# Kernel optimization log

Hardware: AMD Instinct MI355X
Metric: run time of the kernel (lower is better)

Reference implementation:

```python
import jax, jax.numpy as jnp
import numpy as np
import itertools

D_MODEL = 1024
TEMP = 0.3


def _hypercube(n):
    # all 2^n corners of {-1,+1}^n, matching generate_hypercube(n)
    return jnp.asarray(np.array(list(itertools.product([-1.0, 1.0], repeat=n)), dtype=np.float32))


def setup_inputs() -> dict:
    key = jax.random.key(0)
    ks = jax.random.split(key, 12)
    B, T, D = 8, 4096, D_MODEL
    s = 0.02
    return {
        "x": jax.random.normal(ks[0], (B, T, D), dtype=jnp.float32),
        "codes_l1": _hypercube(3),   # (8, 3)
        "codes_l2": _hypercube(6),   # (64, 6)
        "w_to_l1": jax.random.normal(ks[1], (D, 3), dtype=jnp.float32) * s,
        "w_from_l1": jax.random.normal(ks[2], (3, D), dtype=jnp.float32) * s,
        "w_to_l2": jax.random.normal(ks[3], (D, 6), dtype=jnp.float32) * s,
        "w_from_l2": jax.random.normal(ks[4], (6, D), dtype=jnp.float32) * s,
        "w_to_l3u": jax.random.normal(ks[5], (D, 6), dtype=jnp.float32) * s,
        "w_to_l3l": jax.random.normal(ks[6], (D, 6), dtype=jnp.float32) * s,
        "w_from_l3": jax.random.normal(ks[7], (12, D), dtype=jnp.float32) * s,
        "w_gate": jax.random.normal(ks[8], (D, 3), dtype=jnp.float32) * s,
        "b_gate": jnp.zeros((3,), dtype=jnp.float32),
        "temp_l1": jnp.log(jnp.float32(TEMP)),
        "temp_l2": jnp.log(jnp.float32(TEMP * 0.7)),
        "temp_l3": jnp.log(jnp.float32(TEMP * 0.5)),
        "scale_l1": jnp.float32(0.1),
        "scale_l2": jnp.float32(0.05),
        "scale_l3": jnp.float32(0.02),
    }


def _soft_quantize(z, codes, temp_log):
    # z: (B, T, n); codes: (K, n) -> (B, T, n)
    temp = jnp.clip(jnp.exp(temp_log), 0.01, 5.0)
    # Euclidean cdist: (B, T, K)
    dists = jnp.sqrt(jnp.sum(jnp.square(z[..., None, :] - codes), axis=-1))
    weights = jax.nn.softmax(-dists / temp, axis=-1)
    return weights @ codes


def reference(x, codes_l1, codes_l2, w_to_l1, w_from_l1, w_to_l2, w_from_l2,
              w_to_l3u, w_to_l3l, w_from_l3, w_gate, b_gate,
              temp_l1, temp_l2, temp_l3, scale_l1, scale_l2, scale_l3):
    # gate uses detached x
    gate = jax.nn.softmax(jax.lax.stop_gradient(x) @ w_gate + b_gate, axis=-1)  # (B,T,3)

    # Level 1: Z2^3
    q1 = _soft_quantize(x @ w_to_l1, codes_l1, temp_l1)
    out_l1 = q1 @ w_from_l1

    # Level 2: Z2^6
    q2 = _soft_quantize(x @ w_to_l2, codes_l2, temp_l2)
    out_l2 = q2 @ w_from_l2

    # Level 3: Z2^12 = two Z2^6 halves
    q3u = _soft_quantize(x @ w_to_l3u, codes_l2, temp_l3)
    q3l = _soft_quantize(x @ w_to_l3l, codes_l2, temp_l3)
    out_l3 = jnp.concatenate([q3u, q3l], axis=-1) @ w_from_l3

    out = (gate[..., 0:1] * scale_l1 * out_l1
           + gate[..., 1:2] * scale_l2 * out_l2
           + gate[..., 2:3] * scale_l3 * out_l3)
    gate_means = jnp.mean(gate, axis=(0, 1))  # stats dict analogue: (3,)
    return x + out, gate_means
```

## Files before the change

kernel.cpp:

```cpp
#include <hip/hip_runtime.h>
#include <stdint.h>


#define DM 1024
#define TPB 64
#define OUT_OFF ((size_t)33554432)
#define NTOK 32768
#define NSLOT 32
#define WSA_OFF 32768

typedef float f32x4 __attribute__((ext_vector_type(4)));
typedef short bf16x8 __attribute__((ext_vector_type(8)));

typedef const __attribute__((address_space(1))) unsigned int* gas1_t;
typedef __attribute__((address_space(3))) unsigned int* las3_t;

__device__ __forceinline__ void gl_lds16(const void* g, void* l){
  __builtin_amdgcn_global_load_lds((gas1_t)g, (las3_t)l, 16, 0, 0);
}

__device__ __forceinline__ short f2bf(float f){
  unsigned u = __builtin_bit_cast(unsigned, f);
  unsigned r = u + 0x7fffu + ((u >> 16) & 1u);
  return (short)(r >> 16);
}

template<int NB>
__device__ __forceinline__ void softq(const float* z, float invt, float* q){
  constexpr int K = 1 << NB;
  float d[K];
  float dmin = 3.4e38f;
#pragma unroll
  for (int j = 0; j < K; ++j){
    float acc = 0.f;
#pragma unroll
    for (int i = 0; i < NB; ++i){
      float c = ((j >> (NB-1-i)) & 1) ? 1.f : -1.f;
      float t = z[i] - c;
      acc = fmaf(t, t, acc);
    }
    float dj = sqrtf(acc);
    d[j] = dj;
    dmin = fminf(dmin, dj);
  }
  float S = 0.f;
  float s1[NB];
#pragma unroll
  for (int i = 0; i < NB; ++i) s1[i] = 0.f;
#pragma unroll
  for (int j = 0; j < K; ++j){
    float wj = __expf((dmin - d[j]) * invt);
    S += wj;
#pragma unroll
    for (int i = 0; i < NB; ++i)
      if ((j >> (NB-1-i)) & 1) s1[i] += wj;
  }
  float rS = 1.f / S;
#pragma unroll
  for (int i = 0; i < NB; ++i) q[i] = 2.f * s1[i] * rS - 1.f;
}

__global__ __launch_bounds__(256) void pack_kernel(
    const float* __restrict__ w_to_l1,  const float* __restrict__ w_to_l2,
    const float* __restrict__ w_to_l3u, const float* __restrict__ w_to_l3l,
    const float* __restrict__ w_gate,
    const float* __restrict__ w_from_l1, const float* __restrict__ w_from_l2,
    const float* __restrict__ w_from_l3,
    short* __restrict__ wsF, float* __restrict__ wsA)
{
  int base = blockIdx.x*4096 + threadIdx.x*16;
#pragma unroll
  for (int q = 0; q < 16; ++q){
    int e = base + q;
    float v;
    if (e < 32768){
      int s  = e >> 10;
      int nf = (e >> 9) & 1;
      int ll = (e >> 3) & 63;
      int j  = e & 7;
      int k  = s*32 + ((ll >> 4) << 3) + j;
      int n  = nf*16 + (ll & 15);
      if      (n < 3)  v = w_gate  [k*3 + n];
      else if (n < 6)  v = w_to_l1 [k*3 + (n-3)];
      else if (n < 12) v = w_to_l2 [k*6 + (n-6)];
      else if (n < 18) v = w_to_l3u[k*6 + (n-12)];
      else if (n < 24) v = w_to_l3l[k*6 + (n-18)];
      else             v = 0.f;
    } else {
      int e2  = e - 32768;
      int f   = e2 / 384;
      int rem = e2 - f*384;
      int ll  = rem >> 3;
      int j   = e2 & 7;
      int k   = ((ll >> 4) << 3) + j;
      int dd  = f*16 + (ll & 15);
      if      (k < 3)  v = w_from_l1[k*DM + dd];
      else if (k < 9)  v = w_from_l2[(k-3)*DM + dd];
      else if (k < 21) v = w_from_l3[(k-9)*DM + dd];
      else             v = 0.f;
    }
    wsF[e] = f2bf(v);
  }
  if (blockIdx.x == 0){
    wsA[threadIdx.x]       = 0.f;
    wsA[threadIdx.x + 256] = 0.f;
  }
}

__global__ __launch_bounds__(256, 2) void hq7_kernel(
    const float* __restrict__ x, const short* __restrict__ wsF,
    const float* __restrict__ b_gate,
    const float* __restrict__ t1p, const float* __restrict__ t2p, const float* __restrict__ t3p,
    const float* __restrict__ s1p, const float* __restrict__ s2p, const float* __restrict__ s3p,
    float* __restrict__ wsA, float* __restrict__ out)
{
  __shared__ alignas(16) char smem[80576];
  float* C   = reinterpret_cast<float*>(smem + 49152);
  float* P   = reinterpret_cast<float*>(smem + 66560);
  short* V16 = reinterpret_cast<short*>(smem + 75264);
  float* GS  = reinterpret_cast<float*>(smem + 80384);

  const int tid  = threadIdx.x;
  const int l    = tid & 63;
  const int wv   = tid >> 6;
  const int kg   = l >> 4;
  const int ln16 = l & 15;
  const int tb   = blockIdx.x * TPB;

  {
    f32x4 acc0 = {0.f,0.f,0.f,0.f}, acc1 = {0.f,0.f,0.f,0.f};
    const int lr0 = l >> 5;
    const int cbp = l & 31;
#pragma unroll
    for (int i = 0; i < 8; ++i){
      int lr = i*2 + lr0;
      gl_lds16(x + (size_t)(tb + wv*16 + lr)*DM + (cbp ^ (lr & 7))*4,
               smem + wv*16384 + i*1024 + l*16);
    }
#pragma unroll
    for (int t = 0; t < 8; ++t){
      const int buf = t & 1;
      bf16x8 bfr[8];
#pragma unroll
      for (int s2 = 0; s2 < 8; ++s2)
        bfr[s2] = *reinterpret_cast<const bf16x8*>(&wsF[(t*8 + s2)*512 + l*8]);
      __builtin_amdgcn_sched_barrier(0);
      if (t < 7){
#pragma unroll
        for (int i = 0; i < 8; ++i){
          int lr = i*2 + lr0;
          gl_lds16(x + (size_t)(tb + wv*16 + lr)*DM + (t+1)*128 + (cbp ^ (lr & 7))*4,
                   smem + wv*16384 + (buf^1)*8192 + i*1024 + l*16);
        }
        asm volatile("s_waitcnt vmcnt(8)" ::: "memory");
      } else {
        asm volatile("s_waitcnt vmcnt(0)" ::: "memory");
      }
      const char* abase = smem + wv*16384 + buf*8192 + ln16*512;
#pragma unroll
      for (int s = 0; s < 4; ++s){
        float4 xa = *reinterpret_cast<const float4*>(abase + ((s*8 + kg*2 + 0) ^ (ln16 & 7))*16);
        float4 xb = *reinterpret_cast<const float4*>(abase + ((s*8 + kg*2 + 1) ^ (ln16 & 7))*16);
        bf16x8 af;
        af[0]=f2bf(xa.x); af[1]=f2bf(xa.y); af[2]=f2bf(xa.z); af[3]=f2bf(xa.w);
        af[4]=f2bf(xb.x); af[5]=f2bf(xb.y); af[6]=f2bf(xb.z); af[7]=f2bf(xb.w);
        acc0 = __builtin_amdgcn_mfma_f32_16x16x32_bf16(af, bfr[s*2+0], acc0, 0, 0, 0);
        acc1 = __builtin_amdgcn_mfma_f32_16x16x32_bf16(af, bfr[s*2+1], acc1, 0, 0, 0);
      }
    }
#pragma unroll
    for (int r = 0; r < 4; ++r){
      int row = wv*16 + kg*4 + r;
      P[row*34 + ln16]      = acc0[r];
      P[row*34 + 16 + ln16] = acc1[r];
    }
  }
  __syncthreads();

  const short* wsFC = wsF + 32768;
  bf16x8 bwc0={0,0,0,0,0,0,0,0}, bwc1=bwc0, bwc2=bwc0, bwc3=bwc0;
  {
#pragma unroll
    for (int j = 0; j < 4; ++j){
      int lr = j*4 + (l >> 4);
      gl_lds16(x + (size_t)(tb + wv*16 + lr)*DM + ((l & 15) ^ (lr & 7))*4,
               smem + wv*12288 + j*1024 + l*16);
    }
    if (kg < 3){
      bwc0 = *reinterpret_cast<const bf16x8*>(&wsFC[(0*4+0)*384 + l*8]);
      bwc1 = *reinterpret_cast<const bf16x8*>(&wsFC[(0*4+1)*384 + l*8]);
      bwc2 = *reinterpret_cast<const bf16x8*>(&wsFC[(0*4+2)*384 + l*8]);
      bwc3 = *reinterpret_cast<const bf16x8*>(&wsFC[(0*4+3)*384 + l*8]);
    }
#pragma unroll
    for (int j = 0; j < 4; ++j){
      int lr = j*4 + (l >> 4);
      gl_lds16(x + (size_t)(tb + wv*16 + lr)*DM + 64 + ((l & 15) ^ (lr & 7))*4,
               smem + wv*12288 + 4096 + j*1024 + l*16);
    }
  }

  float qv[6] = {0,0,0,0,0,0};
  float myscale = 0.f;
  float sg0 = 0.f, sg1 = 0.f, sg2 = 0.f;
  {
    const int t = l;
    const int base = (wv == 3) ? 0 : 6 + wv*6;
    float z[6];
#pragma unroll
    for (int i = 0; i < 6; ++i) z[i] = P[t*34 + base + i];
    if (wv == 3){
      float invt1 = 1.f / fminf(fmaxf(__expf(t1p[0]), 0.01f), 5.0f);
      float g0l = z[0] + b_gate[0];
      float g1l = z[1] + b_gate[1];
      float g2l = z[2] + b_gate[2];
      float m  = fmaxf(g0l, fmaxf(g1l, g2l));
      float e0 = __expf(g0l - m), e1 = __expf(g1l - m), e2 = __expf(g2l - m);
      float rs = 1.f / (e0 + e1 + e2);
      float g0 = e0*rs, g1 = e1*rs, g2 = e2*rs;
      GS[t*3+0] = g0 * s1p[0];
      GS[t*3+1] = g1 * s2p[0];
      GS[t*3+2] = g2 * s3p[0];
      myscale   = g0 * s1p[0];
      float z1[3] = {z[3], z[4], z[5]};
      softq<3>(z1, invt1, qv);
      sg0 = g0; sg1 = g1; sg2 = g2;
#pragma unroll
      for (int mm = 1; mm < 64; mm <<= 1){
        sg0 += __shfl_xor(sg0, mm, 64);
        sg1 += __shfl_xor(sg1, mm, 64);
        sg2 += __shfl_xor(sg2, mm, 64);
      }
    } else {
      float tl = (wv == 0) ? t2p[0] : t3p[0];
      float invt = 1.f / fminf(fmaxf(__expf(tl), 0.01f), 5.0f);
      softq<6>(z, invt, qv);
    }
  }
  __syncthreads();

  {
    const int t = l;
    if (wv == 3){
#pragma unroll
      for (int i = 0; i < 3; ++i) V16[t*40 + i] = f2bf(myscale * qv[i]);
      V16[t*40 + 21] = 0; V16[t*40 + 22] = 0; V16[t*40 + 23] = 0;
    } else {
      float sc = GS[t*3 + ((wv == 0) ? 1 : 2)];
      int voff = 3 + wv*6;
#pragma unroll
      for (int i = 0; i < 6; ++i) V16[t*40 + voff + i] = f2bf(sc * qv[i]);
    }
  }
  __syncthreads();

  bf16x8 aV = {0,0,0,0,0,0,0,0};
  if (kg < 3)
    aV = *reinterpret_cast<const bf16x8*>(&V16[(wv*16 + ln16)*40 + kg*8]);
  const f32x4 z4 = {0.f,0.f,0.f,0.f};
  const int rl = l >> 2;
  const int cs = l & 3;

#pragma unroll
  for (int c = 0; c < 16; ++c){
    if (c == 0 || c == 15) asm volatile("s_waitcnt vmcnt(4)" ::: "memory");
    else                   asm volatile("s_waitcnt vmcnt(8)" ::: "memory");
    __builtin_amdgcn_sched_barrier(0);
    {
      f32x4 d0 = __builtin_amdgcn_mfma_f32_16x16x32_bf16(aV, bwc0, z4, 0, 0, 0);
      f32x4 d1 = __builtin_amdgcn_mfma_f32_16x16x32_bf16(aV, bwc1, z4, 0, 0, 0);
      f32x4 d2 = __builtin_amdgcn_mfma_f32_16x16x32_bf16(aV, bwc2, z4, 0, 0, 0);
      f32x4 d3 = __builtin_amdgcn_mfma_f32_16x16x32_bf16(aV, bwc3, z4, 0, 0, 0);
#pragma unroll
      for (int r = 0; r < 4; ++r){
        int rowb = (wv*16 + kg*4 + r)*68;
        C[rowb +  0 + ln16] = d0[r];
        C[rowb + 16 + ln16] = d1[r];
        C[rowb + 32 + ln16] = d2[r];
        C[rowb + 48 + ln16] = d3[r];
      }
    }
    __builtin_amdgcn_sched_barrier(0);
    bf16x8 bwn0 = bwc0, bwn1 = bwc1, bwn2 = bwc2, bwn3 = bwc3;
    if (c < 15 && kg < 3){
      bwn0 = *reinterpret_cast<const bf16x8*>(&wsFC[((c+1)*4+0)*384 + l*8]);
      bwn1 = *reinterpret_cast<const bf16x8*>(&wsFC[((c+1)*4+1)*384 + l*8]);
      bwn2 = *reinterpret_cast<const bf16x8*>(&wsFC[((c+1)*4+2)*384 + l*8]);
      bwn3 = *reinterpret_cast<const bf16x8*>(&wsFC[((c+1)*4+3)*384 + l*8]);
    }
    __builtin_amdgcn_sched_barrier(0);
    if (c < 14){
#pragma unroll
      for (int j = 0; j < 4; ++j){
        int lr = j*4 + (l >> 4);
        gl_lds16(x + (size_t)(tb + wv*16 + lr)*DM + (c+2)*64 + ((l & 15) ^ (lr & 7))*4,
                 smem + wv*12288 + ((c+2)%3)*4096 + j*1024 + l*16);
      }
    }
    __builtin_amdgcn_sched_barrier(0);
    asm volatile("s_waitcnt lgkmcnt(0)" ::: "memory");
    __builtin_amdgcn_sched_barrier(0);
#pragma unroll
    for (int q = 0; q < 4; ++q){
      int bi = cs + 4*q;
      f32x4 xv = *reinterpret_cast<const f32x4*>(
          smem + wv*12288 + (c%3)*4096 + rl*256 + ((bi ^ (rl & 7)))*16);
      f32x4 cv = *reinterpret_cast<const f32x4*>(&C[(wv*16 + rl)*68 + bi*4]);
      f32x4 ov = xv + cv;
      *reinterpret_cast<f32x4*>(&out[(size_t)(tb + wv*16 + rl)*DM + c*64 + bi*4]) = ov;
    }
    bwc0 = bwn0; bwc1 = bwn1; bwc2 = bwn2; bwc3 = bwn3;
  }

  if (wv == 3 && l == 0){
    float* slot = wsA + (blockIdx.x & (NSLOT-1))*16;
    atomicAdd(slot + 0, sg0);
    atomicAdd(slot + 1, sg1);
    atomicAdd(slot + 2, sg2);
  }
}

__global__ void finalize_kernel(const float* __restrict__ wsA, float* __restrict__ out){
  if (threadIdx.x < 3){
    float s = 0.f;
    for (int j = 0; j < NSLOT; ++j) s += wsA[j*16 + threadIdx.x];
    out[OUT_OFF + threadIdx.x] = s * (1.f / (float)NTOK);
  }
}

extern "C" void kernel_launch(void* const* d_in, const int* in_sizes, int n_in,
                              void* d_out, int out_size, void* d_ws, size_t ws_size,
                              hipStream_t stream){
  (void)in_sizes; (void)n_in; (void)ws_size; (void)out_size;
  const float* x         = (const float*)d_in[0];
  const float* w_to_l1   = (const float*)d_in[3];
  const float* w_from_l1 = (const float*)d_in[4];
  const float* w_to_l2   = (const float*)d_in[5];
  const float* w_from_l2 = (const float*)d_in[6];
  const float* w_to_l3u  = (const float*)d_in[7];
  const float* w_to_l3l  = (const float*)d_in[8];
  const float* w_from_l3 = (const float*)d_in[9];
  const float* w_gate    = (const float*)d_in[10];
  const float* b_gate    = (const float*)d_in[11];
  const float* t1 = (const float*)d_in[12];
  const float* t2 = (const float*)d_in[13];
  const float* t3 = (const float*)d_in[14];
  const float* s1 = (const float*)d_in[15];
  const float* s2 = (const float*)d_in[16];
  const float* s3 = (const float*)d_in[17];
  float* out  = (float*)d_out;
  short* wsF  = (short*)d_ws;
  float* wsA  = (float*)d_ws + WSA_OFF;

  pack_kernel<<<dim3(14), dim3(256), 0, stream>>>(
      w_to_l1, w_to_l2, w_to_l3u, w_to_l3l, w_gate,
      w_from_l1, w_from_l2, w_from_l3, wsF, wsA);
  hq7_kernel<<<dim3(512), dim3(256), 0, stream>>>(
      x, wsF, b_gate, t1, t2, t3, s1, s2, s3, wsA, out);
  finalize_kernel<<<dim3(1), dim3(64), 0, stream>>>(wsA, out);
}
```

Measured before the change: 79.44 us.

## Make each wave self-contained to drop block barriers and shrink LDS

Each wave now owns a private 16 KB LDS region holding its x staging, projection results, quantized vectors and output tile. The soft-quantize work is spread across the four 16-lane groups of one wave, and the gate scales are passed between groups with shuffles instead of shared memory, so all three __syncthreads are removed. The x prefetch for the output phase changes from a triple buffer to a double buffer that is refilled after the current chunk has been consumed, cutting LDS to 64 KB per block and allowing more blocks per CU. In exchange the refill is issued later, which leaves less time to hide its latency, and more atomics are issued for the gate means.

```diff
diff --git a/kernel.cpp b/kernel.cpp
--- a/kernel.cpp
+++ b/kernel.cpp
@@ -107,25 +107,32 @@
   }
 }
 
-__global__ __launch_bounds__(256, 2) void hq7_kernel(
+__global__ __launch_bounds__(256, 2) void hq8_kernel(
     const float* __restrict__ x, const short* __restrict__ wsF,
     const float* __restrict__ b_gate,
     const float* __restrict__ t1p, const float* __restrict__ t2p, const float* __restrict__ t3p,
     const float* __restrict__ s1p, const float* __restrict__ s2p, const float* __restrict__ s3p,
     float* __restrict__ wsA, float* __restrict__ out)
 {
-  __shared__ alignas(16) char smem[80576];
-  float* C   = reinterpret_cast<float*>(smem + 49152);
-  float* P   = reinterpret_cast<float*>(smem + 66560);
-  short* V16 = reinterpret_cast<short*>(smem + 75264);
-  float* GS  = reinterpret_cast<float*>(smem + 80384);
+  __shared__ alignas(16) char smem[65536];
 
   const int tid  = threadIdx.x;
   const int l    = tid & 63;
   const int wv   = tid >> 6;
   const int kg   = l >> 4;
   const int ln16 = l & 15;
-  const int tb   = blockIdx.x * TPB;
+  const int tokBase = blockIdx.x * TPB + wv*16;
+
+  char*  W  = smem + wv*16384;
+  float* Cw = reinterpret_cast<float*>(W + 8192);
+  float* Pw = reinterpret_cast<float*>(W + 12544);
+  short* Vw = reinterpret_cast<short*>(W + 14720);
+
+  const float invt1 = 1.f / fminf(fmaxf(__expf(t1p[0]), 0.01f), 5.0f);
+  const float invt2 = 1.f / fminf(fmaxf(__expf(t2p[0]), 0.01f), 5.0f);
+  const float invt3 = 1.f / fminf(fmaxf(__expf(t3p[0]), 0.01f), 5.0f);
+  const float s1v = s1p[0], s2v = s2p[0], s3v = s3p[0];
+  const float bg0 = b_gate[0], bg1 = b_gate[1], bg2 = b_gate[2];
 
   {
     f32x4 acc0 = {0.f,0.f,0.f,0.f}, acc1 = {0.f,0.f,0.f,0.f};
@@ -134,8 +141,8 @@
 #pragma unroll
     for (int i = 0; i < 8; ++i){
       int lr = i*2 + lr0;
-      gl_lds16(x + (size_t)(tb + wv*16 + lr)*DM + (cbp ^ (lr & 7))*4,
-               smem + wv*16384 + i*1024 + l*16);
+      gl_lds16(x + (size_t)(tokBase + lr)*DM + (cbp ^ (lr & 7))*4,
+               W + i*1024 + l*16);
     }
 #pragma unroll
     for (int t = 0; t < 8; ++t){
@@ -149,14 +156,14 @@
 #pragma unroll
         for (int i = 0; i < 8; ++i){
           int lr = i*2 + lr0;
-          gl_lds16(x + (size_t)(tb + wv*16 + lr)*DM + (t+1)*128 + (cbp ^ (lr & 7))*4,
-                   smem + wv*16384 + (buf^1)*8192 + i*1024 + l*16);
+          gl_lds16(x + (size_t)(tokBase + lr)*DM + (t+1)*128 + (cbp ^ (lr & 7))*4,
+                   W + (buf^1)*8192 + i*1024 + l*16);
         }
         asm volatile("s_waitcnt vmcnt(8)" ::: "memory");
       } else {
         asm volatile("s_waitcnt vmcnt(0)" ::: "memory");
       }
-      const char* abase = smem + wv*16384 + buf*8192 + ln16*512;
+      const char* abase = W + buf*8192 + ln16*512;
 #pragma unroll
       for (int s = 0; s < 4; ++s){
         float4 xa = *reinterpret_cast<const float4*>(abase + ((s*8 + kg*2 + 0) ^ (ln16 & 7))*16);
@@ -170,12 +177,11 @@
     }
 #pragma unroll
     for (int r = 0; r < 4; ++r){
-      int row = wv*16 + kg*4 + r;
-      P[row*34 + ln16]      = acc0[r];
-      P[row*34 + 16 + ln16] = acc1[r];
-    }
-  }
-  __syncthreads();
+      int row = kg*4 + r;
+      Pw[row*34 + ln16]      = acc0[r];
+      Pw[row*34 + 16 + ln16] = acc1[r];
+    }
+  }
 
   const short* wsFC = wsF + 32768;
   bf16x8 bwc0={0,0,0,0,0,0,0,0}, bwc1=bwc0, bwc2=bwc0, bwc3=bwc0;
@@ -183,80 +189,74 @@
 #pragma unroll
     for (int j = 0; j < 4; ++j){
       int lr = j*4 + (l >> 4);
-      gl_lds16(x + (size_t)(tb + wv*16 + lr)*DM + ((l & 15) ^ (lr & 7))*4,
-               smem + wv*12288 + j*1024 + l*16);
+      gl_lds16(x + (size_t)(tokBase + lr)*DM + ((l & 15) ^ (lr & 7))*4,
+               W + j*1024 + l*16);
     }
     if (kg < 3){
-      bwc0 = *reinterpret_cast<const bf16x8*>(&wsFC[(0*4+0)*384 + l*8]);
-      bwc1 = *reinterpret_cast<const bf16x8*>(&wsFC[(0*4+1)*384 + l*8]);
-      bwc2 = *reinterpret_cast<const bf16x8*>(&wsFC[(0*4+2)*384 + l*8]);
-      bwc3 = *reinterpret_cast<const bf16x8*>(&wsFC[(0*4+3)*384 + l*8]);
+      bwc0 = *reinterpret_cast<const bf16x8*>(&wsFC[0*384 + l*8]);
+      bwc1 = *reinterpret_cast<const bf16x8*>(&wsFC[1*384 + l*8]);
+      bwc2 = *reinterpret_cast<const bf16x8*>(&wsFC[2*384 + l*8]);
+      bwc3 = *reinterpret_cast<const bf16x8*>(&wsFC[3*384 + l*8]);
     }
 #pragma unroll
     for (int j = 0; j < 4; ++j){
       int lr = j*4 + (l >> 4);
-      gl_lds16(x + (size_t)(tb + wv*16 + lr)*DM + 64 + ((l & 15) ^ (lr & 7))*4,
-               smem + wv*12288 + 4096 + j*1024 + l*16);
+      gl_lds16(x + (size_t)(tokBase + lr)*DM + 64 + ((l & 15) ^ (lr & 7))*4,
+               W + 4096 + j*1024 + l*16);
     }
   }
 
   float qv[6] = {0,0,0,0,0,0};
-  float myscale = 0.f;
+  float myscale = 0.f, g1s2v = 0.f, g2s3v = 0.f;
   float sg0 = 0.f, sg1 = 0.f, sg2 = 0.f;
   {
-    const int t = l;
-    const int base = (wv == 3) ? 0 : 6 + wv*6;
+    const int t  = ln16;
+    const int gi = kg;
+    const int base = (gi == 3) ? 0 : 6 + gi*6;
     float z[6];
 #pragma unroll
-    for (int i = 0; i < 6; ++i) z[i] = P[t*34 + base + i];
-    if (wv == 3){
-      float invt1 = 1.f / fminf(fmaxf(__expf(t1p[0]), 0.01f), 5.0f);
-      float g0l = z[0] + b_gate[0];
-      float g1l = z[1] + b_gate[1];
-      float g2l = z[2] + b_gate[2];
+    for (int i = 0; i < 6; ++i) z[i] = Pw[t*34 + base + i];
+    if (gi == 3){
+      float g0l = z[0] + bg0;
+      float g1l = z[1] + bg1;
+      float g2l = z[2] + bg2;
       float m  = fmaxf(g0l, fmaxf(g1l, g2l));
       float e0 = __expf(g0l - m), e1 = __expf(g1l - m), e2 = __expf(g2l - m);
       float rs = 1.f / (e0 + e1 + e2);
       float g0 = e0*rs, g1 = e1*rs, g2 = e2*rs;
-      GS[t*3+0] = g0 * s1p[0];
-      GS[t*3+1] = g1 * s2p[0];
-      GS[t*3+2] = g2 * s3p[0];
-      myscale   = g0 * s1p[0];
+      myscale = g0 * s1v;
+      g1s2v   = g1 * s2v;
+      g2s3v   = g2 * s3v;
       float z1[3] = {z[3], z[4], z[5]};
       softq<3>(z1, invt1, qv);
       sg0 = g0; sg1 = g1; sg2 = g2;
 #pragma unroll
-      for (int mm = 1; mm < 64; mm <<= 1){
+      for (int mm = 1; mm < 16; mm <<= 1){
         sg0 += __shfl_xor(sg0, mm, 64);
         sg1 += __shfl_xor(sg1, mm, 64);
         sg2 += __shfl_xor(sg2, mm, 64);
       }
     } else {
-      float tl = (wv == 0) ? t2p[0] : t3p[0];
-      float invt = 1.f / fminf(fmaxf(__expf(tl), 0.01f), 5.0f);
+      float invt = (gi == 0) ? invt2 : invt3;
       softq<6>(z, invt, qv);
     }
-  }
-  __syncthreads();
-
-  {
-    const int t = l;
-    if (wv == 3){
-#pragma unroll
-      for (int i = 0; i < 3; ++i) V16[t*40 + i] = f2bf(myscale * qv[i]);
-      V16[t*40 + 21] = 0; V16[t*40 + 22] = 0; V16[t*40 + 23] = 0;
+    float gs1 = __shfl(g1s2v, 48 + t, 64);
+    float gs2 = __shfl(g2s3v, 48 + t, 64);
+    if (gi == 3){
+#pragma unroll
+      for (int i = 0; i < 3; ++i) Vw[t*40 + i] = f2bf(myscale * qv[i]);
+      Vw[t*40 + 21] = 0; Vw[t*40 + 22] = 0; Vw[t*40 + 23] = 0;
     } else {
-      float sc = GS[t*3 + ((wv == 0) ? 1 : 2)];
-      int voff = 3 + wv*6;
-#pragma unroll
-      for (int i = 0; i < 6; ++i) V16[t*40 + voff + i] = f2bf(sc * qv[i]);
-    }
-  }
-  __syncthreads();
+      float sc = (gi == 0) ? gs1 : gs2;
+      int voff = 3 + gi*6;
+#pragma unroll
+      for (int i = 0; i < 6; ++i) Vw[t*40 + voff + i] = f2bf(sc * qv[i]);
+    }
+  }
 
   bf16x8 aV = {0,0,0,0,0,0,0,0};
   if (kg < 3)
-    aV = *reinterpret_cast<const bf16x8*>(&V16[(wv*16 + ln16)*40 + kg*8]);
+    aV = *reinterpret_cast<const bf16x8*>(&Vw[ln16*40 + kg*8]);
   const f32x4 z4 = {0.f,0.f,0.f,0.f};
   const int rl = l >> 2;
   const int cs = l & 3;
@@ -273,11 +273,11 @@
       f32x4 d3 = __builtin_amdgcn_mfma_f32_16x16x32_bf16(aV, bwc3, z4, 0, 0, 0);
 #pragma unroll
       for (int r = 0; r < 4; ++r){
-        int rowb = (wv*16 + kg*4 + r)*68;
-        C[rowb +  0 + ln16] = d0[r];
-        C[rowb + 16 + ln16] = d1[r];
-        C[rowb + 32 + ln16] = d2[r];
-        C[rowb + 48 + ln16] = d3[r];
+        int rowb = (kg*4 + r)*68;
+        Cw[rowb +  0 + ln16] = d0[r];
+        Cw[rowb + 16 + ln16] = d1[r];
+        Cw[rowb + 32 + ln16] = d2[r];
+        Cw[rowb + 48 + ln16] = d3[r];
       }
     }
     __builtin_amdgcn_sched_barrier(0);
@@ -289,31 +289,31 @@
       bwn3 = *reinterpret_cast<const bf16x8*>(&wsFC[((c+1)*4+3)*384 + l*8]);
     }
     __builtin_amdgcn_sched_barrier(0);
-    if (c < 14){
-#pragma unroll
-      for (int j = 0; j < 4; ++j){
-        int lr = j*4 + (l >> 4);
-        gl_lds16(x + (size_t)(tb + wv*16 + lr)*DM + (c+2)*64 + ((l & 15) ^ (lr & 7))*4,
-                 smem + wv*12288 + ((c+2)%3)*4096 + j*1024 + l*16);
-      }
-    }
-    __builtin_amdgcn_sched_barrier(0);
     asm volatile("s_waitcnt lgkmcnt(0)" ::: "memory");
     __builtin_amdgcn_sched_barrier(0);
 #pragma unroll
     for (int q = 0; q < 4; ++q){
       int bi = cs + 4*q;
       f32x4 xv = *reinterpret_cast<const f32x4*>(
-          smem + wv*12288 + (c%3)*4096 + rl*256 + ((bi ^ (rl & 7)))*16);
-      f32x4 cv = *reinterpret_cast<const f32x4*>(&C[(wv*16 + rl)*68 + bi*4]);
+          W + (c & 1)*4096 + rl*256 + ((bi ^ (rl & 7)))*16);
+      f32x4 cv = *reinterpret_cast<const f32x4*>(&Cw[rl*68 + bi*4]);
       f32x4 ov = xv + cv;
-      *reinterpret_cast<f32x4*>(&out[(size_t)(tb + wv*16 + rl)*DM + c*64 + bi*4]) = ov;
+      *reinterpret_cast<f32x4*>(&out[(size_t)(tokBase + rl)*DM + c*64 + bi*4]) = ov;
+    }
+    __builtin_amdgcn_sched_barrier(0);
+    if (c < 14){
+#pragma unroll
+      for (int j = 0; j < 4; ++j){
+        int lr = j*4 + (l >> 4);
+        gl_lds16(x + (size_t)(tokBase + lr)*DM + (c+2)*64 + ((l & 15) ^ (lr & 7))*4,
+                 W + (c & 1)*4096 + j*1024 + l*16);
+      }
     }
     bwc0 = bwn0; bwc1 = bwn1; bwc2 = bwn2; bwc3 = bwn3;
   }
 
-  if (wv == 3 && l == 0){
-    float* slot = wsA + (blockIdx.x & (NSLOT-1))*16;
+  if (l == 48){
+    float* slot = wsA + ((blockIdx.x*4 + wv) & (NSLOT-1))*16;
     atomicAdd(slot + 0, sg0);
     atomicAdd(slot + 1, sg1);
     atomicAdd(slot + 2, sg2);
@@ -355,7 +355,7 @@
   pack_kernel<<<dim3(14), dim3(256), 0, stream>>>(
       w_to_l1, w_to_l2, w_to_l3u, w_to_l3l, w_gate,
       w_from_l1, w_from_l2, w_from_l3, wsF, wsA);
-  hq7_kernel<<<dim3(512), dim3(256), 0, stream>>>(
+  hq8_kernel<<<dim3(512), dim3(256), 0, stream>>>(
       x, wsF, b_gate, t1, t2, t3, s1, s2, s3, wsA, out);
   finalize_kernel<<<dim3(1), dim3(64), 0, stream>>>(wsA, out);
 }
```

Measured after the change: 81.03 us. No clear change (+2.0%).
